# Kernel optimization log

Hardware: AMD Instinct MI355X
Metric: run time of the kernel (lower is better)

The kernel has to match this reference:

```python
import jax, jax.numpy as jnp
import numpy as np

B, S, E, H = 2, 4096, 768, 12
D = E // H  # head_dim = 64
SCALE = D ** -0.5
NEG = -1e9


def setup_inputs() -> dict:
    key = jax.random.key(0)
    ks = jax.random.split(key, 10)
    init = lambda k, shape: jax.random.normal(k, shape, dtype=jnp.float32) * (shape[-1] ** -0.5)
    x = jax.random.normal(ks[0], (B, S, E), dtype=jnp.float32)
    attention_mask = jnp.zeros((B, 1, S, S), dtype=jnp.float32)
    # additive causal mask: 0 on/below diagonal, -1e9 above
    causal = jnp.where(jnp.tril(jnp.ones((S, S), dtype=bool)), 0.0, NEG).astype(jnp.float32)
    causal_attention_mask = causal[None, None]
    return {
        "x": x,
        "attention_mask": attention_mask,
        "causal_attention_mask": causal_attention_mask,
        "Wq": init(ks[1], (E, E)), "bq": jnp.zeros((E,), jnp.float32),
        "Wk": init(ks[2], (E, E)), "bk": jnp.zeros((E,), jnp.float32),
        "Wv": init(ks[3], (E, E)), "bv": jnp.zeros((E,), jnp.float32),
        "Wo": init(ks[4], (E, E)), "bo": jnp.zeros((E,), jnp.float32),
    }


def _split_heads(t):
    # [B,S,E] -> [B,H,S,D]
    return t.reshape(B, S, H, D).transpose(0, 2, 1, 3)


def reference(x, attention_mask, causal_attention_mask, Wq, bq, Wk, bk, Wv, bv, Wo, bo):
    q = _split_heads(x @ Wq.T + bq)
    k = _split_heads(x @ Wk.T + bk)
    v = _split_heads(x @ Wv.T + bv)
    mask = attention_mask + causal_attention_mask  # [B,1,S,S]
    scores = jnp.einsum("bhqd,bhkd->bhqk", q, k) * SCALE + mask
    probs = jax.nn.softmax(scores.astype(jnp.float32), axis=-1).astype(q.dtype)
    out = jnp.einsum("bhqk,bhkd->bhqd", probs, v)
    out = out.transpose(0, 2, 1, 3).reshape(B, S, E)
    return out @ Wo.T + bo
```

## Files before the change

### kernel.cpp

```cpp
#include <hip/hip_runtime.h>
#include <hip/hip_bf16.h>
#include <stdint.h>

#define B_ 2
#define S_ 4096
#define E_ 768
#define H_ 12
#define D_ 64
#define M_TOT (B_*S_)
#define NQKV (3*E_)

typedef __attribute__((ext_vector_type(8)))  short bf16x8;
typedef __attribute__((ext_vector_type(4)))  float f32x4;
typedef __attribute__((ext_vector_type(16))) float f32x16;
typedef unsigned short u16;
typedef unsigned int   u32;

__device__ __forceinline__ u16 f2bf(float f) {
  __hip_bfloat16 h = __float2bfloat16(f);
  return *reinterpret_cast<u16*>(&h);
}

__device__ __forceinline__ u32 cvtpk(float lo, float hi) {
  u32 r;
  asm("v_cvt_pk_bf16_f32 %0, %1, %2" : "=v"(r) : "v"(lo), "v"(hi));
  return r;
}

#define GLDS(gp, lp) __builtin_amdgcn_global_load_lds( \
    (const __attribute__((address_space(1))) void*)(gp), \
    (__attribute__((address_space(3))) void*)(lp), 16, 0, 0)


__global__ void k_cast_x(const float* __restrict__ x, u16* __restrict__ xb) {
  int i = blockIdx.x * blockDim.x + threadIdx.x;
  float4 v = reinterpret_cast<const float4*>(x)[i];
  ushort4 o;
  o.x = f2bf(v.x); o.y = f2bf(v.y); o.z = f2bf(v.z); o.w = f2bf(v.w);
  reinterpret_cast<ushort4*>(xb)[i] = o;
}

#define QSCALE 0.1803368801111573f

__global__ void k_pack_wqkv(const float* __restrict__ Wq, const float* __restrict__ Wk,
                            const float* __restrict__ Wv, const float* __restrict__ bq,
                            const float* __restrict__ bk, const float* __restrict__ bv,
                            u16* __restrict__ wqkv, float* __restrict__ bqkv) {
  int i = blockIdx.x * blockDim.x + threadIdx.x;
  int base = i * 4;
  int n = base / E_;
  int k = base % E_;
  const float* src; float sc;
  if (n < E_)        { src = Wq + (size_t)n*E_ + k;          sc = QSCALE; }
  else if (n < 2*E_) { src = Wk + (size_t)(n-E_)*E_ + k;     sc = 1.f; }
  else               { src = Wv + (size_t)(n-2*E_)*E_ + k;   sc = 1.f; }
  float4 v = *reinterpret_cast<const float4*>(src);
  ushort4 o;
  o.x = f2bf(v.x*sc); o.y = f2bf(v.y*sc); o.z = f2bf(v.z*sc); o.w = f2bf(v.w*sc);
  reinterpret_cast<ushort4*>(wqkv)[i] = o;
  if (i < NQKV) {
    float b = (i < E_) ? bq[i]*QSCALE : (i < 2*E_) ? bk[i-E_] : bv[i-2*E_];
    bqkv[i] = b;
  }
}

__global__ void k_cast_wo(const float* __restrict__ Wo, u16* __restrict__ wo) {
  int i = blockIdx.x * blockDim.x + threadIdx.x;
  float4 v = reinterpret_cast<const float4*>(Wo)[i];
  ushort4 o;
  o.x = f2bf(v.x); o.y = f2bf(v.y); o.z = f2bf(v.z); o.w = f2bf(v.w);
  reinterpret_cast<ushort4*>(wo)[i] = o;
}


template<int MODE>
__global__ __launch_bounds__(256)
void k_gemm(const u16* __restrict__ A, const u16* __restrict__ W,
            const float* __restrict__ bias,
            u16* __restrict__ dq, u16* __restrict__ dk, u16* __restrict__ dv,
            float* __restrict__ fout)
{
  __shared__ u16 As[128*64];
  __shared__ u16 Ws[128*64];
  const int tid  = threadIdx.x;
  const int lane = tid & 63, wave = tid >> 6;
  const int m0 = blockIdx.x * 128;
  const int n0 = blockIdx.y * 128;
  const int g  = lane >> 4, cc = lane & 15;
  const int wr = (wave >> 1) * 64, wc = (wave & 1) * 64;
  const int srow = lane >> 3;
  const int scol = (lane & 7) * 8;

  f32x4 acc[4][4];
  #pragma unroll
  for (int m = 0; m < 4; ++m)
    #pragma unroll
    for (int n = 0; n < 4; ++n) acc[m][n] = (f32x4){0.f,0.f,0.f,0.f};

  for (int k0 = 0; k0 < E_; k0 += 64) {
    __syncthreads();
    #pragma unroll
    for (int i = 0; i < 4; ++i) {
      const int r0 = (i*4 + wave) * 8;
      GLDS(A + (size_t)(m0 + r0 + srow)*E_ + k0 + scol, As + r0*64);
      GLDS(W + (size_t)(n0 + r0 + srow)*E_ + k0 + scol, Ws + r0*64);
    }
    __syncthreads();
    #pragma unroll
    for (int kk = 0; kk < 64; kk += 32) {
      bf16x8 af[4], bfr[4];
      #pragma unroll
      for (int m = 0; m < 4; ++m)
        af[m] = *reinterpret_cast<const bf16x8*>(As + (wr + m*16 + cc)*64 + kk + g*8);
      #pragma unroll
      for (int n = 0; n < 4; ++n)
        bfr[n] = *reinterpret_cast<const bf16x8*>(Ws + (wc + n*16 + cc)*64 + kk + g*8);
      #pragma unroll
      for (int m = 0; m < 4; ++m)
        #pragma unroll
        for (int n = 0; n < 4; ++n)
          acc[m][n] = __builtin_amdgcn_mfma_f32_16x16x32_bf16(af[m], bfr[n], acc[m][n], 0, 0, 0);
    }
  }

  #pragma unroll
  for (int n = 0; n < 4; ++n) {
    const int colg = n0 + wc + n*16 + cc;
    const float bb = bias[colg];
    if (MODE == 0) {
      const int which = colg / E_;
      const int nn = colg % E_;
      const int h = nn >> 6, d = nn & 63;
      #pragma unroll
      for (int m = 0; m < 4; ++m)
        #pragma unroll
        for (int j = 0; j < 4; ++j) {
          const int row = m0 + wr + m*16 + g*4 + j;
          const int b = row >> 12, s = row & (S_-1);
          const u16 val = f2bf(acc[m][n][j] + bb);
          if (which == 0)       dq[(((size_t)b*H_ + h)*S_ + s)*D_ + d] = val;
          else if (which == 1)  dk[(((size_t)b*H_ + h)*S_ + s)*D_ + d] = val;
          else                  dv[(((size_t)b*H_ + h)*D_ + d)*S_ + s] = val;
        }
    } else {
      #pragma unroll
      for (int m = 0; m < 4; ++m)
        #pragma unroll
        for (int j = 0; j < 4; ++j) {
          const int row = m0 + wr + m*16 + g*4 + j;
          fout[(size_t)row*E_ + colg] = acc[m][n][j] + bb;
        }
    }
  }
}


__global__ __launch_bounds__(256, 3)
void k_attn(const u16* __restrict__ Qb, const u16* __restrict__ Kb,
            const u16* __restrict__ Vtg, u16* __restrict__ AO)
{
  __shared__ u16 Ks[2][32*128];
  __shared__ u16 Vs[2][32*128];
  const int tid = threadIdx.x, lane = tid & 63, w = tid >> 6;

  const int L  = blockIdx.x;
  const int kk = L >> 8;
  const int j  = L & 255;
  const int x  = j & 7;
  const int c  = j >> 3;
  const int bh = x*3 + kk;
  const int u  = c >> 1;
  int qt;
  if (kk == 0)      qt = c;
  else if (kk == 1) qt = (c & 1) ? ((u < 15) ? 14 - u : 15) : 31 - u;
  else              qt = (c & 1) ? ((u < 15) ? 31 - u : 0)  : 16 - u;

  const int q0 = qt * 128;
  const int ntiles = 2*qt + 2;

  const size_t kbase = (size_t)bh * S_ * D_;
  const size_t vbase = (size_t)bh * D_ * S_;
  const int hi = lane >> 5, l31 = lane & 31;
  const int swz = (lane & 15) << 4;
  const int qg = q0 + w*32 + l31;

  int stA[2], stB[2];
  #pragma unroll
  for (int i = 0; i < 2; ++i) {
    const int jj = 2*w + i;
    const int row = jj*4 + (lane >> 4);
    const int gb = ((lane & 15) * 16) ^ ((row & 15) << 4);
    stA[i] = row + 32*(gb >> 7);
    stB[i] = (gb & 127) >> 1;
  }

  bf16x8 qf[4];
  #pragma unroll
  for (int ds = 0; ds < 4; ++ds)
    qf[ds] = *reinterpret_cast<const bf16x8*>(Qb + kbase + (size_t)qg*D_ + ds*16 + hi*8);

  float m_run = -INFINITY, l_run = 0.f;
  f32x16 o0, o1;
  #pragma unroll
  for (int r = 0; r < 16; ++r) { o0[r] = 0.f; o1[r] = 0.f; }

#define STAGE(buf, kv0_) do { \
    _Pragma("unroll") \
    for (int i = 0; i < 2; ++i) { \
      GLDS(Kb  + kbase + (size_t)((kv0_) + stA[i])*D_ + stB[i], &Ks[buf][(2*w+i)*512]); \
      GLDS(Vtg + vbase + (size_t)stA[i]*S_ + (kv0_) + stB[i],   &Vs[buf][(2*w+i)*512]); \
    } } while(0)

  int cur = 0;
  STAGE(0, 0);

  for (int t = 0; t < ntiles; ++t) {
    const int kv0 = t * 64;
    asm volatile("s_waitcnt vmcnt(0)" ::: "memory");
    __builtin_amdgcn_s_barrier();
    asm volatile("" ::: "memory");
    if (t + 1 < ntiles) STAGE(cur ^ 1, (t+1)*64);

    const u16* bK = Ks[cur];
    const u16* bV = Vs[cur];

    f32x16 s0, s1;
    #pragma unroll
    for (int r = 0; r < 16; ++r) { s0[r] = 0.f; s1[r] = 0.f; }
    __builtin_amdgcn_s_setprio(1);
    #pragma unroll
    for (int ds = 0; ds < 4; ++ds) {
      const int off = ((32*ds + 16*hi) ^ swz) >> 1;
      bf16x8 a0 = *reinterpret_cast<const bf16x8*>(bK + l31*128 + off);
      bf16x8 a1 = *reinterpret_cast<const bf16x8*>(bK + l31*128 + (off ^ 64));
      s0 = __builtin_amdgcn_mfma_f32_32x32x16_bf16(a0, qf[ds], s0, 0, 0, 0);
      s1 = __builtin_amdgcn_mfma_f32_32x32x16_bf16(a1, qf[ds], s1, 0, 0, 0);
    }
    __builtin_amdgcn_s_setprio(0);

    if (t >= ntiles - 2) {
      #pragma unroll
      for (int r = 0; r < 16; ++r) {
        const int kvl = kv0 + (r&3) + 8*(r>>2) + 4*hi;
        s0[r] = (kvl      > qg) ? -1e30f : s0[r];
        s1[r] = (kvl + 32 > qg) ? -1e30f : s1[r];
      }
    }

    float m4[8];
    #pragma unroll
    for (int i = 0; i < 4; ++i)
      m4[i] = fmaxf(fmaxf(s0[4*i], s0[4*i+1]), fmaxf(s0[4*i+2], s0[4*i+3]));
    #pragma unroll
    for (int i = 0; i < 4; ++i)
      m4[4+i] = fmaxf(fmaxf(s1[4*i], s1[4*i+1]), fmaxf(s1[4*i+2], s1[4*i+3]));
    float mx = fmaxf(fmaxf(fmaxf(m4[0], m4[1]), fmaxf(m4[2], m4[3])),
                     fmaxf(fmaxf(m4[4], m4[5]), fmaxf(m4[6], m4[7])));
    mx = fmaxf(mx, __shfl_xor(mx, 32));

    if (!__all(mx <= m_run + 8.0f)) {
      const float mnew  = fmaxf(m_run, mx);
      const float alpha = exp2f(m_run - mnew);
      m_run = mnew;
      l_run *= alpha;
      #pragma unroll
      for (int r = 0; r < 16; ++r) { o0[r] *= alpha; o1[r] *= alpha; }
    }

    #pragma unroll
    for (int r = 0; r < 16; ++r) s0[r] = exp2f(s0[r] - m_run);
    #pragma unroll
    for (int r = 0; r < 16; ++r) s1[r] = exp2f(s1[r] - m_run);
    float t4[8];
    #pragma unroll
    for (int i = 0; i < 4; ++i)
      t4[i] = (s0[4*i] + s0[4*i+1]) + (s0[4*i+2] + s0[4*i+3]);
    #pragma unroll
    for (int i = 0; i < 4; ++i)
      t4[4+i] = (s1[4*i] + s1[4*i+1]) + (s1[4*i+2] + s1[4*i+3]);
    float sum = ((t4[0]+t4[1]) + (t4[2]+t4[3])) + ((t4[4]+t4[5]) + (t4[6]+t4[7]));
    sum += __shfl_xor(sum, 32);
    l_run += sum;

    u32 c16[16];
    #pragma unroll
    for (int i = 0; i < 8; ++i) {
      c16[i]   = cvtpk(s0[2*i], s0[2*i+1]);
      c16[8+i] = cvtpk(s1[2*i], s1[2*i+1]);
    }

    #pragma unroll
    for (int ks = 0; ks < 4; ++ks) {
      const int cb = (ks>>1)*8 + (ks&1)*4;
      u32 x0 = c16[cb],   y0 = c16[cb+2];
      u32 x1 = c16[cb+1], y1 = c16[cb+3];
      asm volatile("v_permlane32_swap_b32 %0, %1" : "+v"(x0), "+v"(y0));
      asm volatile("v_permlane32_swap_b32 %0, %1" : "+v"(x1), "+v"(y1));
      union { u32 u[4]; bf16x8 v; } pf;
      pf.u[0] = x0; pf.u[1] = x1; pf.u[2] = y0; pf.u[3] = y1;
      const int voff = ((32*ks + 16*hi) ^ swz) >> 1;
      bf16x8 v0 = *reinterpret_cast<const bf16x8*>(bV + l31*128 + voff);
      bf16x8 v1 = *reinterpret_cast<const bf16x8*>(bV + l31*128 + (voff ^ 64));
      __builtin_amdgcn_s_setprio(1);
      o0 = __builtin_amdgcn_mfma_f32_32x32x16_bf16(v0, pf.v, o0, 0, 0, 0);
      o1 = __builtin_amdgcn_mfma_f32_32x32x16_bf16(v1, pf.v, o1, 0, 0, 0);
      __builtin_amdgcn_s_setprio(0);
    }

    asm volatile("" ::: "memory");
    __builtin_amdgcn_s_barrier();
    cur ^= 1;
  }
#undef STAGE

  const int b = bh / H_, h = bh % H_;
  const float inv = 1.0f / l_run;
  u16* dst = AO + ((size_t)b*S_ + qg)*E_ + h*64;
  #pragma unroll
  for (int aa = 0; aa < 4; ++aa) {
    ushort4 wv;
    wv.x = f2bf(o0[4*aa+0]*inv); wv.y = f2bf(o0[4*aa+1]*inv);
    wv.z = f2bf(o0[4*aa+2]*inv); wv.w = f2bf(o0[4*aa+3]*inv);
    *reinterpret_cast<ushort4*>(dst + aa*8 + hi*4) = wv;
  }
  #pragma unroll
  for (int aa = 0; aa < 4; ++aa) {
    ushort4 wv;
    wv.x = f2bf(o1[4*aa+0]*inv); wv.y = f2bf(o1[4*aa+1]*inv);
    wv.z = f2bf(o1[4*aa+2]*inv); wv.w = f2bf(o1[4*aa+3]*inv);
    *reinterpret_cast<ushort4*>(dst + 32 + aa*8 + hi*4) = wv;
  }
}


extern "C" void kernel_launch(void* const* d_in, const int* in_sizes, int n_in,
                              void* d_out, int out_size, void* d_ws, size_t ws_size,
                              hipStream_t stream) {
  const float* x  = (const float*)d_in[0];
  const float* Wq = (const float*)d_in[3];
  const float* bq = (const float*)d_in[4];
  const float* Wk = (const float*)d_in[5];
  const float* bk = (const float*)d_in[6];
  const float* Wv = (const float*)d_in[7];
  const float* bv = (const float*)d_in[8];
  const float* Wo = (const float*)d_in[9];
  const float* bo = (const float*)d_in[10];
  float* out = (float*)d_out;

  const size_t SZ_X   = (size_t)M_TOT * E_ * 2;
  const size_t SZ_WQKV= (size_t)NQKV * E_ * 2;
  const size_t SZ_WO  = (size_t)E_ * E_ * 2;
  const size_t SZ_B   = (size_t)NQKV * 4;
  char* w = (char*)d_ws;
  u16*   xb   = (u16*)(w);
  u16*   wqkv = (u16*)(w + SZ_X);
  u16*   wob  = (u16*)(w + SZ_X + SZ_WQKV);
  float* bqkv = (float*)(w + SZ_X + SZ_WQKV + SZ_WO);
  char*  w2   = w + SZ_X + SZ_WQKV + SZ_WO + SZ_B;
  u16* Qb = (u16*)(w2);
  u16* Kb = (u16*)(w2 + SZ_X);
  u16* Vb = (u16*)(w2 + 2*SZ_X);
  u16* AO = (u16*)(w2 + 3*SZ_X);

  k_cast_x  <<<6144, 256, 0, stream>>>(x, xb);
  k_pack_wqkv<<<1728, 256, 0, stream>>>(Wq, Wk, Wv, bq, bk, bv, wqkv, bqkv);
  k_cast_wo <<<576,  256, 0, stream>>>(Wo, wob);

  dim3 gq(64, 18);
  k_gemm<0><<<gq, 256, 0, stream>>>(xb, wqkv, bqkv, Qb, Kb, Vb, nullptr);

  k_attn<<<768, 256, 0, stream>>>(Qb, Kb, Vb, AO);

  dim3 go(64, 6);
  k_gemm<1><<<go, 256, 0, stream>>>(AO, wob, bo, nullptr, nullptr, nullptr, out);
}
```

Before: 233.6 us.

## Fuse prep kernels, swizzle GEMM grid, reorder attention tiles with max3 and lazy rescale

Merges the three cast/pack kernels into one launch and remaps GEMM blocks onto an XCD-aware 1D swizzled grid. The output-projection GEMM now uses 64-wide N tiles so it launches more blocks. The attention kernel processes the two diagonal (masked) KV tiles first, so the running max is seeded from them. It folds the max subtraction into the MFMA accumulator init, uses v_max3 for the row-max reduction, and rescales only when the new max exceeds the running max by more than 24. Together these aim to cut launch overhead, improve L2 locality and trim softmax ALU work. The higher rescale threshold carries some risk of fp32 range issues.

```diff
diff --git a/kernel.cpp b/kernel.cpp
--- a/kernel.cpp
+++ b/kernel.cpp
@@ -27,49 +27,58 @@
   return r;
 }
 
+__device__ __forceinline__ float max3f(float a, float b, float c) {
+  float d;
+  asm("v_max3_f32 %0, %1, %2, %3" : "=v"(d) : "v"(a), "v"(b), "v"(c));
+  return d;
+}
+
 #define GLDS(gp, lp) __builtin_amdgcn_global_load_lds( \
     (const __attribute__((address_space(1))) void*)(gp), \
     (__attribute__((address_space(3))) void*)(lp), 16, 0, 0)
 
-
-__global__ void k_cast_x(const float* __restrict__ x, u16* __restrict__ xb) {
-  int i = blockIdx.x * blockDim.x + threadIdx.x;
-  float4 v = reinterpret_cast<const float4*>(x)[i];
-  ushort4 o;
-  o.x = f2bf(v.x); o.y = f2bf(v.y); o.z = f2bf(v.z); o.w = f2bf(v.w);
-  reinterpret_cast<ushort4*>(xb)[i] = o;
-}
-
 #define QSCALE 0.1803368801111573f
 
-__global__ void k_pack_wqkv(const float* __restrict__ Wq, const float* __restrict__ Wk,
-                            const float* __restrict__ Wv, const float* __restrict__ bq,
-                            const float* __restrict__ bk, const float* __restrict__ bv,
-                            u16* __restrict__ wqkv, float* __restrict__ bqkv) {
-  int i = blockIdx.x * blockDim.x + threadIdx.x;
-  int base = i * 4;
-  int n = base / E_;
-  int k = base % E_;
-  const float* src; float sc;
-  if (n < E_)        { src = Wq + (size_t)n*E_ + k;          sc = QSCALE; }
-  else if (n < 2*E_) { src = Wk + (size_t)(n-E_)*E_ + k;     sc = 1.f; }
-  else               { src = Wv + (size_t)(n-2*E_)*E_ + k;   sc = 1.f; }
-  float4 v = *reinterpret_cast<const float4*>(src);
-  ushort4 o;
-  o.x = f2bf(v.x*sc); o.y = f2bf(v.y*sc); o.z = f2bf(v.z*sc); o.w = f2bf(v.w*sc);
-  reinterpret_cast<ushort4*>(wqkv)[i] = o;
-  if (i < NQKV) {
-    float b = (i < E_) ? bq[i]*QSCALE : (i < 2*E_) ? bk[i-E_] : bv[i-2*E_];
-    bqkv[i] = b;
-  }
-}
-
-__global__ void k_cast_wo(const float* __restrict__ Wo, u16* __restrict__ wo) {
-  int i = blockIdx.x * blockDim.x + threadIdx.x;
-  float4 v = reinterpret_cast<const float4*>(Wo)[i];
-  ushort4 o;
-  o.x = f2bf(v.x); o.y = f2bf(v.y); o.z = f2bf(v.z); o.w = f2bf(v.w);
-  reinterpret_cast<ushort4*>(wo)[i] = o;
+
+__global__ void k_prep(const float* __restrict__ x,
+                       const float* __restrict__ Wq, const float* __restrict__ Wk,
+                       const float* __restrict__ Wv, const float* __restrict__ bq,
+                       const float* __restrict__ bk, const float* __restrict__ bv,
+                       const float* __restrict__ Wo,
+                       u16* __restrict__ xb, u16* __restrict__ wqkv,
+                       float* __restrict__ bqkv, u16* __restrict__ wob)
+{
+  const int bid = blockIdx.x;
+  if (bid < 6144) {
+    int i = bid * 256 + threadIdx.x;
+    float4 v = reinterpret_cast<const float4*>(x)[i];
+    ushort4 o;
+    o.x = f2bf(v.x); o.y = f2bf(v.y); o.z = f2bf(v.z); o.w = f2bf(v.w);
+    reinterpret_cast<ushort4*>(xb)[i] = o;
+  } else if (bid < 6144 + 1728) {
+    int i = (bid - 6144) * 256 + threadIdx.x;
+    int base = i * 4;
+    int n = base / E_;
+    int k = base % E_;
+    const float* src; float sc;
+    if (n < E_)        { src = Wq + (size_t)n*E_ + k;        sc = QSCALE; }
+    else if (n < 2*E_) { src = Wk + (size_t)(n-E_)*E_ + k;   sc = 1.f; }
+    else               { src = Wv + (size_t)(n-2*E_)*E_ + k; sc = 1.f; }
+    float4 v = *reinterpret_cast<const float4*>(src);
+    ushort4 o;
+    o.x = f2bf(v.x*sc); o.y = f2bf(v.y*sc); o.z = f2bf(v.z*sc); o.w = f2bf(v.w*sc);
+    reinterpret_cast<ushort4*>(wqkv)[i] = o;
+    if (i < NQKV) {
+      float b = (i < E_) ? bq[i]*QSCALE : (i < 2*E_) ? bk[i-E_] : bv[i-2*E_];
+      bqkv[i] = b;
+    }
+  } else {
+    int i = (bid - 7872) * 256 + threadIdx.x;
+    float4 v = reinterpret_cast<const float4*>(Wo)[i];
+    ushort4 o;
+    o.x = f2bf(v.x); o.y = f2bf(v.y); o.z = f2bf(v.z); o.w = f2bf(v.w);
+    reinterpret_cast<ushort4*>(wob)[i] = o;
+  }
 }
 
 
@@ -80,22 +89,26 @@
             u16* __restrict__ dq, u16* __restrict__ dk, u16* __restrict__ dv,
             float* __restrict__ fout)
 {
+  constexpr int BN = (MODE == 0) ? 128 : 64;
+  constexpr int NF = BN / 32;
+  constexpr int CPX = (MODE == 0) ? 144 : 96;
   __shared__ u16 As[128*64];
-  __shared__ u16 Ws[128*64];
+  __shared__ u16 Ws[BN*64];
   const int tid  = threadIdx.x;
   const int lane = tid & 63, wave = tid >> 6;
-  const int m0 = blockIdx.x * 128;
-  const int n0 = blockIdx.y * 128;
+  const int sw = (blockIdx.x & 7) * CPX + (blockIdx.x >> 3);
+  const int m0 = (sw & 63) * 128;
+  const int n0 = (sw >> 6) * BN;
   const int g  = lane >> 4, cc = lane & 15;
-  const int wr = (wave >> 1) * 64, wc = (wave & 1) * 64;
+  const int wr = (wave >> 1) * 64, wc = (wave & 1) * (BN/2);
   const int srow = lane >> 3;
   const int scol = (lane & 7) * 8;
 
-  f32x4 acc[4][4];
+  f32x4 acc[4][NF];
   #pragma unroll
   for (int m = 0; m < 4; ++m)
     #pragma unroll
-    for (int n = 0; n < 4; ++n) acc[m][n] = (f32x4){0.f,0.f,0.f,0.f};
+    for (int n = 0; n < NF; ++n) acc[m][n] = (f32x4){0.f,0.f,0.f,0.f};
 
   for (int k0 = 0; k0 < E_; k0 += 64) {
     __syncthreads();
@@ -103,28 +116,32 @@
     for (int i = 0; i < 4; ++i) {
       const int r0 = (i*4 + wave) * 8;
       GLDS(A + (size_t)(m0 + r0 + srow)*E_ + k0 + scol, As + r0*64);
+    }
+    #pragma unroll
+    for (int i = 0; i < BN/32; ++i) {
+      const int r0 = (i*4 + wave) * 8;
       GLDS(W + (size_t)(n0 + r0 + srow)*E_ + k0 + scol, Ws + r0*64);
     }
     __syncthreads();
     #pragma unroll
     for (int kk = 0; kk < 64; kk += 32) {
-      bf16x8 af[4], bfr[4];
+      bf16x8 af[4], bfr[NF];
       #pragma unroll
       for (int m = 0; m < 4; ++m)
         af[m] = *reinterpret_cast<const bf16x8*>(As + (wr + m*16 + cc)*64 + kk + g*8);
       #pragma unroll
-      for (int n = 0; n < 4; ++n)
+      for (int n = 0; n < NF; ++n)
         bfr[n] = *reinterpret_cast<const bf16x8*>(Ws + (wc + n*16 + cc)*64 + kk + g*8);
       #pragma unroll
       for (int m = 0; m < 4; ++m)
         #pragma unroll
-        for (int n = 0; n < 4; ++n)
+        for (int n = 0; n < NF; ++n)
           acc[m][n] = __builtin_amdgcn_mfma_f32_16x16x32_bf16(af[m], bfr[n], acc[m][n], 0, 0, 0);
     }
   }
 
   #pragma unroll
-  for (int n = 0; n < 4; ++n) {
+  for (int n = 0; n < NF; ++n) {
     const int colg = n0 + wc + n*16 + cc;
     const float bb = bias[colg];
     if (MODE == 0) {
@@ -176,7 +193,7 @@
   else              qt = (c & 1) ? ((u < 15) ? 31 - u : 0)  : 16 - u;
 
   const int q0 = qt * 128;
-  const int ntiles = 2*qt + 2;
+  const int nt = 2*qt + 2;
 
   const size_t kbase = (size_t)bh * S_ * D_;
   const size_t vbase = (size_t)bh * D_ * S_;
@@ -199,7 +216,7 @@
   for (int ds = 0; ds < 4; ++ds)
     qf[ds] = *reinterpret_cast<const bf16x8*>(Qb + kbase + (size_t)qg*D_ + ds*16 + hi*8);
 
-  float m_run = -INFINITY, l_run = 0.f;
+  float m_run = 0.f, l_run = 0.f;
   f32x16 o0, o1;
   #pragma unroll
   for (int r = 0; r < 16; ++r) { o0[r] = 0.f; o1[r] = 0.f; }
@@ -212,21 +229,26 @@
     } } while(0)
 
   int cur = 0;
-  STAGE(0, 0);
-
-  for (int t = 0; t < ntiles; ++t) {
-    const int kv0 = t * 64;
+  STAGE(0, (nt-2)*64);
+
+  for (int it = 0; it < nt; ++it) {
     asm volatile("s_waitcnt vmcnt(0)" ::: "memory");
     __builtin_amdgcn_s_barrier();
     asm volatile("" ::: "memory");
-    if (t + 1 < ntiles) STAGE(cur ^ 1, (t+1)*64);
+    if (it + 1 < nt) {
+      const int nk = (it + 1 == 1) ? (nt - 1) : (it - 1);
+      STAGE(cur ^ 1, nk * 64);
+    }
+    const int kvt = (it == 0) ? (nt - 2) : ((it == 1) ? (nt - 1) : (it - 2));
+    const int kv0 = kvt * 64;
 
     const u16* bK = Ks[cur];
     const u16* bV = Vs[cur];
 
+    const float minit = (it == 0) ? 0.f : -m_run;
     f32x16 s0, s1;
     #pragma unroll
-    for (int r = 0; r < 16; ++r) { s0[r] = 0.f; s1[r] = 0.f; }
+    for (int r = 0; r < 16; ++r) { s0[r] = minit; s1[r] = minit; }
     __builtin_amdgcn_s_setprio(1);
     #pragma unroll
     for (int ds = 0; ds < 4; ++ds) {
@@ -238,7 +260,7 @@
     }
     __builtin_amdgcn_s_setprio(0);
 
-    if (t >= ntiles - 2) {
+    if (it <= 1) {
       #pragma unroll
       for (int r = 0; r < 16; ++r) {
         const int kvl = kv0 + (r&3) + 8*(r>>2) + 4*hi;
@@ -247,30 +269,43 @@
       }
     }
 
-    float m4[8];
-    #pragma unroll
-    for (int i = 0; i < 4; ++i)
-      m4[i] = fmaxf(fmaxf(s0[4*i], s0[4*i+1]), fmaxf(s0[4*i+2], s0[4*i+3]));
-    #pragma unroll
-    for (int i = 0; i < 4; ++i)
-      m4[4+i] = fmaxf(fmaxf(s1[4*i], s1[4*i+1]), fmaxf(s1[4*i+2], s1[4*i+3]));
-    float mx = fmaxf(fmaxf(fmaxf(m4[0], m4[1]), fmaxf(m4[2], m4[3])),
-                     fmaxf(fmaxf(m4[4], m4[5]), fmaxf(m4[6], m4[7])));
+    float a0_ = max3f(s0[0],  s0[1],  s0[2]);
+    float a1_ = max3f(s0[3],  s0[4],  s0[5]);
+    float a2_ = max3f(s0[6],  s0[7],  s0[8]);
+    float a3_ = max3f(s0[9],  s0[10], s0[11]);
+    float a4_ = max3f(s0[12], s0[13], s0[14]);
+    float a5_ = max3f(s1[0],  s1[1],  s1[2]);
+    float a6_ = max3f(s1[3],  s1[4],  s1[5]);
+    float a7_ = max3f(s1[6],  s1[7],  s1[8]);
+    float a8_ = max3f(s1[9],  s1[10], s1[11]);
+    float a9_ = max3f(s1[12], s1[13], s1[14]);
+    float b0_ = max3f(a0_, a1_, a2_);
+    float b1_ = max3f(a3_, a4_, s0[15]);
+    float b2_ = max3f(a5_, a6_, a7_);
+    float b3_ = max3f(a8_, a9_, s1[15]);
+    float mx  = max3f(b0_, b1_, fmaxf(b2_, b3_));
     mx = fmaxf(mx, __shfl_xor(mx, 32));
 
-    if (!__all(mx <= m_run + 8.0f)) {
-      const float mnew  = fmaxf(m_run, mx);
-      const float alpha = exp2f(m_run - mnew);
-      m_run = mnew;
+    if (it == 0) {
+      m_run = mx;
+      #pragma unroll
+      for (int r = 0; r < 16; ++r) { s0[r] -= mx; s1[r] -= mx; }
+    } else if (!__all(mx <= 24.0f)) {
+      const float mxc   = fmaxf(mx, 0.f);
+      const float alpha = exp2f(-mxc);
+      m_run += mxc;
       l_run *= alpha;
       #pragma unroll
-      for (int r = 0; r < 16; ++r) { o0[r] *= alpha; o1[r] *= alpha; }
-    }
-
-    #pragma unroll
-    for (int r = 0; r < 16; ++r) s0[r] = exp2f(s0[r] - m_run);
-    #pragma unroll
-    for (int r = 0; r < 16; ++r) s1[r] = exp2f(s1[r] - m_run);
+      for (int r = 0; r < 16; ++r) {
+        o0[r] *= alpha; o1[r] *= alpha;
+        s0[r] -= mxc;   s1[r] -= mxc;
+      }
+    }
+    #pragma unroll
+    for (int r = 0; r < 16; ++r) s0[r] = exp2f(s0[r]);
+    #pragma unroll
+    for (int r = 0; r < 16; ++r) s1[r] = exp2f(s1[r]);
+
     float t4[8];
     #pragma unroll
     for (int i = 0; i < 4; ++i)
@@ -362,15 +397,12 @@
   u16* Vb = (u16*)(w2 + 2*SZ_X);
   u16* AO = (u16*)(w2 + 3*SZ_X);
 
-  k_cast_x  <<<6144, 256, 0, stream>>>(x, xb);
-  k_pack_wqkv<<<1728, 256, 0, stream>>>(Wq, Wk, Wv, bq, bk, bv, wqkv, bqkv);
-  k_cast_wo <<<576,  256, 0, stream>>>(Wo, wob);
-
-  dim3 gq(64, 18);
-  k_gemm<0><<<gq, 256, 0, stream>>>(xb, wqkv, bqkv, Qb, Kb, Vb, nullptr);
+  k_prep<<<8448, 256, 0, stream>>>(x, Wq, Wk, Wv, bq, bk, bv, Wo,
+                                   xb, wqkv, bqkv, wob);
+
+  k_gemm<0><<<1152, 256, 0, stream>>>(xb, wqkv, bqkv, Qb, Kb, Vb, nullptr);
 
   k_attn<<<768, 256, 0, stream>>>(Qb, Kb, Vb, AO);
 
-  dim3 go(64, 6);
-  k_gemm<1><<<go, 256, 0, stream>>>(AO, wob, bo, nullptr, nullptr, nullptr, out);
-}
+  k_gemm<1><<<768, 256, 0, stream>>>(AO, wob, bo, nullptr, nullptr, nullptr, out);
+}
```

Measured after the change: 233.5 us. No clear change (-0.0%).
